# Kernel optimization log

Measured on AMD Instinct MI355X. Metric: run time of the kernel, lower is better.

Reference implementation:

```python
import jax, jax.numpy as jnp
import numpy as np

EPS = 1e-5  # matches torch default epsilon


def setup_inputs() -> dict:
    key = jax.random.key(0)
    ks = jax.random.split(key, 7)
    B, S, H = 32, 8192, 128
    return {
        "time_to_maturity": jax.random.uniform(ks[0], (B, S), jnp.float32),
        "log_moneyness": jax.random.normal(ks[1], (B, S), jnp.float32),
        "target_variance": jax.random.uniform(ks[2], (B, S), jnp.float32),
        "W1": jax.random.normal(ks[3], (2, H), jnp.float32) * 0.5,
        "b1": jax.random.normal(ks[4], (H,), jnp.float32) * 0.1,
        "W2": jax.random.normal(ks[5], (H,), jnp.float32) * 0.5,
        "b2": jax.random.normal(ks[6], (1,), jnp.float32) * 0.1,
    }


def reference(time_to_maturity, log_moneyness, target_variance, W1, b1, W2, b2):
    # Upstream surface model: elementwise (t, x) -> total implied variance w > 0.
    def w_fn(t, x):
        h = jnp.tanh(t * W1[0] + x * W1[1] + b1)  # [H]
        return jax.nn.softplus(jnp.dot(h, W2) + b2[0])  # scalar

    w_t_fn = jax.grad(w_fn, argnums=0)
    w_x_fn = jax.grad(w_fn, argnums=1)
    w_xx_fn = jax.grad(w_x_fn, argnums=1)

    tf = time_to_maturity.reshape(-1)   # [N] flattened query points
    xf = log_moneyness.reshape(-1)
    tgt = target_variance.reshape(-1)
    N = tf.shape[0]

    # Diagonal Jacobian entries: replaces the O(N^2) unit-vector autograd loop.
    w = jax.vmap(w_fn)(tf, xf)
    w_t = jax.vmap(w_t_fn)(tf, xf)
    w_x = jax.vmap(w_x_fn)(tf, xf)
    w_xx = jax.vmap(w_xx_fn)(tf, xf)

    percentage_error = (w - tgt) / (tgt + EPS)
    mspe = jnp.sum(percentage_error ** 2)

    calendar = jnp.sum(jnp.maximum(-w_t, 0.0) ** 2)

    # Durrleman butterfly condition g(x)
    g = (1.0 - xf * w_x / (2.0 * w)) ** 2 - (w_x / 4.0) * (1.0 / w + 0.25) + w_xx / 2.0
    butterfly = jnp.sum(jnp.maximum(-g, 0.0) ** 2)

    return jnp.stack([mspe, calendar, butterfly]) / N
```

## Files before the change

kernel.cpp:

```cpp
#include <hip/hip_runtime.h>
#include <cmath>

#define HDIM 128
typedef float f32x2 __attribute__((ext_vector_type(2)));

constexpr float EPSF = 1e-5f;
constexpr float K2L  = 2.8853900817779268f;
constexpr float INVK = 0.34657359027997264f;
constexpr float L2E  = 1.4426950408889634f;
constexpr float LN2  = 0.6931471805599453f;
constexpr float UXXS = -2.0f * INVK * INVK;

__device__ inline float fast_rcp(float x) { return __builtin_amdgcn_rcpf(x); }

__device__ inline float fast_exp2(float x) {
#if __has_builtin(__builtin_amdgcn_exp2f)
    return __builtin_amdgcn_exp2f(x);
#else
    float r; asm("v_exp_f32 %0, %1" : "=v"(r) : "v"(x)); return r;
#endif
}

__device__ inline float fast_log2(float x) {
#if __has_builtin(__builtin_amdgcn_logf)
    return __builtin_amdgcn_logf(x);
#else
    float r; asm("v_log_f32 %0, %1" : "=v"(r) : "v"(x)); return r;
#endif
}

__device__ inline f32x2 splat2(float v) { return (f32x2){v, v}; }

__device__ inline f32x2 pk_fma(f32x2 a, f32x2 b, f32x2 c) {
#if __has_builtin(__builtin_elementwise_fma)
    return __builtin_elementwise_fma(a, b, c);
#else
    f32x2 r; r.x = fmaf(a.x, b.x, c.x); r.y = fmaf(a.y, b.y, c.y); return r;
#endif
}

__device__ inline double wave_reduce(double v) {
    #pragma unroll
    for (int off = 32; off > 0; off >>= 1)
        v += __shfl_down(v, off, 64);
    return v;
}

__device__ inline void point_epilogue(float u, float ut, float ux, float uxxp,
                                      float x, float tgt,
                                      double& mspe, double& cal, double& bfly)
{
    const float q  = fast_exp2(-fabsf(u) * L2E);
    const float rp = fast_rcp(1.f + q);
    const float s  = (u >= 0.f) ? rp : q * rp;
    const float w_log  = fmaxf(u, 0.f) + LN2 * fast_log2(1.f + q);
    const float w_tail = q * fmaf(-0.5f, q, 1.f);
    const float w  = (u < -9.f) ? w_tail : w_log;

    const float utt  = ut * INVK;
    const float uxt  = ux * INVK;
    const float uxxt = uxxp * UXXS;
    const float w_t  = s * utt;
    const float w_x  = s * uxt;
    const float w_xx = fmaf(s * (1.f - s), uxt * uxt, s * uxxt);

    const float pe = (w - tgt) * fast_rcp(tgt + EPSF);
    mspe += (double)pe * (double)pe;

    const float ctm = fmaxf(-w_t, 0.f);
    cal += (double)ctm * (double)ctm;

    const float invw = fast_rcp(w);
    const float a1 = fmaf(-0.5f * x * w_x, invw, 1.f);
    const float g  = fmaf(0.5f, w_xx,
                     fmaf(a1, a1, -0.25f * w_x * (invw + 0.25f)));
    const float btm = fmaxf(-g, 0.f);
    bfly += (double)btm * (double)btm;
}

__global__ __launch_bounds__(256) void surf_loss_main(
    const float* __restrict__ tt, const float* __restrict__ xx,
    const float* __restrict__ tg,
    const float* __restrict__ W1, const float* __restrict__ b1,
    const float* __restrict__ W2, const float* __restrict__ b2,
    double* __restrict__ partials, int N)
{
    __shared__ float4 cs[HDIM];
    __shared__ double sred[3][4];
    const int tid = threadIdx.x;
    for (int i = tid; i < HDIM; i += 256) {
        cs[i] = make_float4(W1[i] * K2L, W1[HDIM + i] * K2L, b1[i] * K2L, W2[i]);
    }
    __syncthreads();
    const float b2v = b2[0];

    double mspe = 0.0, cal = 0.0, bfly = 0.0;

    const int npair = N >> 1;
    const f32x2* __restrict__ tt2 = (const f32x2*)tt;
    const f32x2* __restrict__ xx2 = (const f32x2*)xx;
    const f32x2* __restrict__ tg2 = (const f32x2*)tg;

    for (int p = blockIdx.x * 256 + tid; p < npair; p += gridDim.x * 256) {
        const f32x2 t2 = tt2[p], x2 = xx2[p], g2 = tg2[p];
        f32x2 u2   = splat2(b2v);
        f32x2 ut2  = splat2(0.f);
        f32x2 ux2  = splat2(0.f);
        f32x2 uxx2 = splat2(0.f);
        #pragma unroll 8
        for (int i = 0; i < HDIM; ++i) {
            const float4 c = cs[i];
            f32x2 zp = pk_fma(x2, splat2(c.y), splat2(c.z));
            zp = pk_fma(t2, splat2(c.x), zp);
            f32x2 e2; e2.x = fast_exp2(zp.x); e2.y = fast_exp2(zp.y);
            const f32x2 ep = e2 + splat2(1.f);
            f32x2 r2; r2.x = fast_rcp(ep.x); r2.y = fast_rcp(ep.y);
            const f32x2 th2 = pk_fma(splat2(-2.f), r2, splat2(1.f));
            const f32x2 d2  = pk_fma(-th2, th2, splat2(1.f));
            const f32x2 wd2 = splat2(c.w) * d2;
            u2   = pk_fma(splat2(c.w), th2, u2);
            ut2  = pk_fma(wd2, splat2(c.x), ut2);
            ux2  = pk_fma(wd2, splat2(c.y), ux2);
            const f32x2 wtc = (wd2 * th2) * splat2(c.y);
            uxx2 = pk_fma(wtc, splat2(c.y), uxx2);
        }
        point_epilogue(u2.x, ut2.x, ux2.x, uxx2.x, x2.x, g2.x, mspe, cal, bfly);
        point_epilogue(u2.y, ut2.y, ux2.y, uxx2.y, x2.y, g2.y, mspe, cal, bfly);
    }

    if ((N & 1) && blockIdx.x == 0 && tid == 0) {
        const int idx = N - 1;
        const float t = tt[idx], x = xx[idx], tgt = tg[idx];
        float u = b2v, ut = 0.f, ux = 0.f, uxx = 0.f;
        for (int i = 0; i < HDIM; ++i) {
            const float4 c = cs[i];
            const float zp = fmaf(t, c.x, fmaf(x, c.y, c.z));
            const float e  = fast_exp2(zp);
            const float r  = fast_rcp(e + 1.f);
            const float th = fmaf(-2.f, r, 1.f);
            const float d  = fmaf(-th, th, 1.f);
            const float wd = c.w * d;
            u   = fmaf(c.w, th, u);
            ut  = fmaf(wd, c.x, ut);
            ux  = fmaf(wd, c.y, ux);
            uxx = fmaf(wd * th * c.y, c.y, uxx);
        }
        point_epilogue(u, ut, ux, uxx, x, tgt, mspe, cal, bfly);
    }

    double v0 = wave_reduce(mspe), v1 = wave_reduce(cal), v2 = wave_reduce(bfly);
    const int wid = tid >> 6, lane = tid & 63;
    if (lane == 0) { sred[0][wid] = v0; sred[1][wid] = v1; sred[2][wid] = v2; }
    __syncthreads();
    if (tid == 0) {
        double a = 0, b = 0, c = 0;
        #pragma unroll
        for (int wv = 0; wv < 4; ++wv) { a += sred[0][wv]; b += sred[1][wv]; c += sred[2][wv]; }
        partials[blockIdx.x * 3 + 0] = a;
        partials[blockIdx.x * 3 + 1] = b;
        partials[blockIdx.x * 3 + 2] = c;
    }
}

__global__ __launch_bounds__(256) void surf_loss_final(
    const double* __restrict__ partials, int nblocks, float* __restrict__ out, int N)
{
    const int tid = threadIdx.x;
    double a = 0, b = 0, c = 0;
    for (int i = tid; i < nblocks; i += 256) {
        a += partials[i * 3 + 0];
        b += partials[i * 3 + 1];
        c += partials[i * 3 + 2];
    }
    a = wave_reduce(a); b = wave_reduce(b); c = wave_reduce(c);
    __shared__ double sred[3][4];
    const int wid = tid >> 6, lane = tid & 63;
    if (lane == 0) { sred[0][wid] = a; sred[1][wid] = b; sred[2][wid] = c; }
    __syncthreads();
    if (tid == 0) {
        const double inv = 1.0 / (double)N;
        double s0 = 0, s1 = 0, s2 = 0;
        #pragma unroll
        for (int wv = 0; wv < 4; ++wv) { s0 += sred[0][wv]; s1 += sred[1][wv]; s2 += sred[2][wv]; }
        out[0] = (float)(s0 * inv);
        out[1] = (float)(s1 * inv);
        out[2] = (float)(s2 * inv);
    }
}

extern "C" void kernel_launch(void* const* d_in, const int* in_sizes, int n_in,
                              void* d_out, int out_size, void* d_ws, size_t ws_size,
                              hipStream_t stream) {
    const float* tt = (const float*)d_in[0];
    const float* xx = (const float*)d_in[1];
    const float* tg = (const float*)d_in[2];
    const float* W1 = (const float*)d_in[3];
    const float* b1 = (const float*)d_in[4];
    const float* W2 = (const float*)d_in[5];
    const float* b2 = (const float*)d_in[6];
    const int N = in_sizes[0];

    const int npair = N >> 1;
    int blocks = (npair + 255) / 256;
    if (blocks < 1) blocks = 1;
    if (blocks > 1024) blocks = 1024;
    while ((size_t)blocks * 3 * sizeof(double) > ws_size && blocks > 1) blocks >>= 1;

    double* partials = (double*)d_ws;
    surf_loss_main<<<blocks, 256, 0, stream>>>(tt, xx, tg, W1, b1, W2, b2, partials, N);
    surf_loss_final<<<1, 256, 0, stream>>>(partials, blocks, (float*)d_out, N);
}
```

Measured before the change: 20.54 us.

## Split hidden dimension across lane pairs and fuse final reduction via atomic counter

Each pair of adjacent lanes now shares two points, with each lane evaluating half of the 128 hidden units for both points, and the partial sums are combined with xor shuffles. This doubles the thread count per point so the grid has more work items per block. The separate final-reduction kernel is replaced by a last-block-done pattern using an atomic counter, with a memset to reset it. The cost is extra shuffles and a memset launch in place of the second kernel launch.

New measurement: 35.89 us. 74.7% more time.

```diff
diff --git a/kernel.cpp b/kernel.cpp
--- a/kernel.cpp
+++ b/kernel.cpp
@@ -78,15 +78,17 @@
     bfly += (double)btm * (double)btm;
 }
 
-__global__ __launch_bounds__(256) void surf_loss_main(
+__global__ __launch_bounds__(256, 4) void surf_loss_fused(
     const float* __restrict__ tt, const float* __restrict__ xx,
     const float* __restrict__ tg,
     const float* __restrict__ W1, const float* __restrict__ b1,
     const float* __restrict__ W2, const float* __restrict__ b2,
-    double* __restrict__ partials, int N)
+    double* __restrict__ partials, unsigned* __restrict__ counter,
+    float* __restrict__ out, int N)
 {
     __shared__ float4 cs[HDIM];
     __shared__ double sred[3][4];
+    __shared__ int lastflag;
     const int tid = threadIdx.x;
     for (int i = tid; i < HDIM; i += 256) {
         cs[i] = make_float4(W1[i] * K2L, W1[HDIM + i] * K2L, b1[i] * K2L, W2[i]);
@@ -96,42 +98,56 @@
 
     double mspe = 0.0, cal = 0.0, bfly = 0.0;
 
-    const int npair = N >> 1;
+    const int Ne = N & ~1;
     const f32x2* __restrict__ tt2 = (const f32x2*)tt;
     const f32x2* __restrict__ xx2 = (const f32x2*)xx;
     const f32x2* __restrict__ tg2 = (const f32x2*)tg;
 
-    for (int p = blockIdx.x * 256 + tid; p < npair; p += gridDim.x * 256) {
-        const f32x2 t2 = tt2[p], x2 = xx2[p], g2 = tg2[p];
-        f32x2 u2   = splat2(b2v);
+    const int h    = tid & 1;
+    const int coff = h << 6;
+
+    for (int g = blockIdx.x * 256 + tid; g < Ne; g += gridDim.x * 256) {
+        const int p = g >> 1;
+        const f32x2 tv = tt2[p], xv = xx2[p], gv = tg2[p];
+        f32x2 u2   = splat2(0.f);
         f32x2 ut2  = splat2(0.f);
         f32x2 ux2  = splat2(0.f);
         f32x2 uxx2 = splat2(0.f);
-        #pragma unroll 8
-        for (int i = 0; i < HDIM; ++i) {
-            const float4 c = cs[i];
-            f32x2 zp = pk_fma(x2, splat2(c.y), splat2(c.z));
-            zp = pk_fma(t2, splat2(c.x), zp);
-            f32x2 e2; e2.x = fast_exp2(zp.x); e2.y = fast_exp2(zp.y);
-            const f32x2 ep = e2 + splat2(1.f);
-            f32x2 r2; r2.x = fast_rcp(ep.x); r2.y = fast_rcp(ep.y);
-            const f32x2 th2 = pk_fma(splat2(-2.f), r2, splat2(1.f));
-            const f32x2 d2  = pk_fma(-th2, th2, splat2(1.f));
-            const f32x2 wd2 = splat2(c.w) * d2;
-            u2   = pk_fma(splat2(c.w), th2, u2);
-            ut2  = pk_fma(wd2, splat2(c.x), ut2);
-            ux2  = pk_fma(wd2, splat2(c.y), ux2);
-            const f32x2 wtc = (wd2 * th2) * splat2(c.y);
+        #pragma unroll 4
+        for (int i = 0; i < HDIM / 2; ++i) {
+            const float4 c = cs[i + coff];
+            const f32x2 z  = pk_fma(tv, splat2(c.x),
+                              pk_fma(xv, splat2(c.y), splat2(c.z)));
+            f32x2 e;  e.x = fast_exp2(z.x); e.y = fast_exp2(z.y);
+            const f32x2 ep = e + splat2(1.f);
+            f32x2 r;  r.x = fast_rcp(ep.x); r.y = fast_rcp(ep.y);
+            const f32x2 th = pk_fma(splat2(-2.f), r, splat2(1.f));
+            const f32x2 d  = pk_fma(-th, th, splat2(1.f));
+            const f32x2 wd = d * splat2(c.w);
+            u2   = pk_fma(th, splat2(c.w), u2);
+            ut2  = pk_fma(wd, splat2(c.x), ut2);
+            ux2  = pk_fma(wd, splat2(c.y), ux2);
+            const f32x2 wt  = wd * th;
+            const f32x2 wtc = wt * splat2(c.y);
             uxx2 = pk_fma(wtc, splat2(c.y), uxx2);
         }
-        point_epilogue(u2.x, ut2.x, ux2.x, uxx2.x, x2.x, g2.x, mspe, cal, bfly);
-        point_epilogue(u2.y, ut2.y, ux2.y, uxx2.y, x2.y, g2.y, mspe, cal, bfly);
+        u2.x   += __shfl_xor(u2.x,   1, 64);  u2.y   += __shfl_xor(u2.y,   1, 64);
+        ut2.x  += __shfl_xor(ut2.x,  1, 64);  ut2.y  += __shfl_xor(ut2.y,  1, 64);
+        ux2.x  += __shfl_xor(ux2.x,  1, 64);  ux2.y  += __shfl_xor(ux2.y,  1, 64);
+        uxx2.x += __shfl_xor(uxx2.x, 1, 64);  uxx2.y += __shfl_xor(uxx2.y, 1, 64);
+        const float u    = (h ? u2.y   : u2.x) + b2v;
+        const float ut   =  h ? ut2.y  : ut2.x;
+        const float ux   =  h ? ux2.y  : ux2.x;
+        const float uxxp =  h ? uxx2.y : uxx2.x;
+        const float xs   =  h ? xv.y   : xv.x;
+        const float tgs  =  h ? gv.y   : gv.x;
+        point_epilogue(u, ut, ux, uxxp, xs, tgs, mspe, cal, bfly);
     }
 
     if ((N & 1) && blockIdx.x == 0 && tid == 0) {
         const int idx = N - 1;
         const float t = tt[idx], x = xx[idx], tgt = tg[idx];
-        float u = b2v, ut = 0.f, ux = 0.f, uxx = 0.f;
+        float u = 0.f, ut = 0.f, ux = 0.f, uxx = 0.f;
         for (int i = 0; i < HDIM; ++i) {
             const float4 c = cs[i];
             const float zp = fmaf(t, c.x, fmaf(x, c.y, c.z));
@@ -145,7 +161,7 @@
             ux  = fmaf(wd, c.y, ux);
             uxx = fmaf(wd * th * c.y, c.y, uxx);
         }
-        point_epilogue(u, ut, ux, uxx, x, tgt, mspe, cal, bfly);
+        point_epilogue(u + b2v, ut, ux, uxx, x, tgt, mspe, cal, bfly);
     }
 
     double v0 = wave_reduce(mspe), v1 = wave_reduce(cal), v2 = wave_reduce(bfly);
@@ -159,32 +175,32 @@
         partials[blockIdx.x * 3 + 0] = a;
         partials[blockIdx.x * 3 + 1] = b;
         partials[blockIdx.x * 3 + 2] = c;
-    }
-}
-
-__global__ __launch_bounds__(256) void surf_loss_final(
-    const double* __restrict__ partials, int nblocks, float* __restrict__ out, int N)
-{
-    const int tid = threadIdx.x;
-    double a = 0, b = 0, c = 0;
-    for (int i = tid; i < nblocks; i += 256) {
-        a += partials[i * 3 + 0];
-        b += partials[i * 3 + 1];
-        c += partials[i * 3 + 2];
-    }
-    a = wave_reduce(a); b = wave_reduce(b); c = wave_reduce(c);
-    __shared__ double sred[3][4];
-    const int wid = tid >> 6, lane = tid & 63;
-    if (lane == 0) { sred[0][wid] = a; sred[1][wid] = b; sred[2][wid] = c; }
+        const unsigned old = __hip_atomic_fetch_add(counter, 1u,
+                                __ATOMIC_ACQ_REL, __HIP_MEMORY_SCOPE_AGENT);
+        lastflag = (old == gridDim.x - 1) ? 1 : 0;
+    }
     __syncthreads();
-    if (tid == 0) {
-        const double inv = 1.0 / (double)N;
-        double s0 = 0, s1 = 0, s2 = 0;
-        #pragma unroll
-        for (int wv = 0; wv < 4; ++wv) { s0 += sred[0][wv]; s1 += sred[1][wv]; s2 += sred[2][wv]; }
-        out[0] = (float)(s0 * inv);
-        out[1] = (float)(s1 * inv);
-        out[2] = (float)(s2 * inv);
+
+    if (lastflag) {
+        double a = 0, b = 0, c = 0;
+        const int nb = (int)gridDim.x;
+        for (int i = tid; i < nb; i += 256) {
+            a += __hip_atomic_load(&partials[i * 3 + 0], __ATOMIC_RELAXED, __HIP_MEMORY_SCOPE_AGENT);
+            b += __hip_atomic_load(&partials[i * 3 + 1], __ATOMIC_RELAXED, __HIP_MEMORY_SCOPE_AGENT);
+            c += __hip_atomic_load(&partials[i * 3 + 2], __ATOMIC_RELAXED, __HIP_MEMORY_SCOPE_AGENT);
+        }
+        a = wave_reduce(a); b = wave_reduce(b); c = wave_reduce(c);
+        if (lane == 0) { sred[0][wid] = a; sred[1][wid] = b; sred[2][wid] = c; }
+        __syncthreads();
+        if (tid == 0) {
+            const double inv = 1.0 / (double)N;
+            double s0 = 0, s1 = 0, s2 = 0;
+            #pragma unroll
+            for (int wv = 0; wv < 4; ++wv) { s0 += sred[0][wv]; s1 += sred[1][wv]; s2 += sred[2][wv]; }
+            out[0] = (float)(s0 * inv);
+            out[1] = (float)(s1 * inv);
+            out[2] = (float)(s2 * inv);
+        }
     }
 }
 
@@ -200,13 +216,15 @@
     const float* b2 = (const float*)d_in[6];
     const int N = in_sizes[0];
 
-    const int npair = N >> 1;
-    int blocks = (npair + 255) / 256;
+    int blocks = (N + 255) / 256;
     if (blocks < 1) blocks = 1;
     if (blocks > 1024) blocks = 1024;
-    while ((size_t)blocks * 3 * sizeof(double) > ws_size && blocks > 1) blocks >>= 1;
-
-    double* partials = (double*)d_ws;
-    surf_loss_main<<<blocks, 256, 0, stream>>>(tt, xx, tg, W1, b1, W2, b2, partials, N);
-    surf_loss_final<<<1, 256, 0, stream>>>(partials, blocks, (float*)d_out, N);
-}
+    while (32 + (size_t)blocks * 3 * sizeof(double) > ws_size && blocks > 1) blocks >>= 1;
+
+    unsigned* counter = (unsigned*)d_ws;
+    double* partials  = (double*)((char*)d_ws + 32);
+
+    hipMemsetAsync(d_ws, 0, 32, stream);
+    surf_loss_fused<<<blocks, 256, 0, stream>>>(tt, xx, tg, W1, b1, W2, b2,
+                                                partials, counter, (float*)d_out, N);
+}
```

## Reformulate tanh-MLP derivative sums in sigmoid form and share one reciprocal per pair

Applied to the files above, without the earlier changes.

Rewrites the hidden-unit loop in terms of r = 1/(1+e^z), using th = 1-2r and 1-th^2 = 4r(1-r). Weight products and the bias sum are precomputed into a second shared-memory table, so the inner loop runs fewer dependent ops. The two reciprocals per point pair become one reciprocal of the product plus two multiplies, cutting transcendental-unit pressure. It also adds an occupancy hint to launch bounds. The risks are overflow or underflow in ep.x*ep.y for large z, extra LDS reads per iteration, and changed rounding.

Result: slower. 21.19 us (+3.1%).

```diff
diff --git a/kernel.cpp b/kernel.cpp
--- a/kernel.cpp
+++ b/kernel.cpp
@@ -6,10 +6,8 @@
 
 constexpr float EPSF = 1e-5f;
 constexpr float K2L  = 2.8853900817779268f;
-constexpr float INVK = 0.34657359027997264f;
 constexpr float L2E  = 1.4426950408889634f;
 constexpr float LN2  = 0.6931471805599453f;
-constexpr float UXXS = -2.0f * INVK * INVK;
 
 __device__ inline float fast_rcp(float x) { return __builtin_amdgcn_rcpf(x); }
 
@@ -46,7 +44,7 @@
     return v;
 }
 
-__device__ inline void point_epilogue(float u, float ut, float ux, float uxxp,
+__device__ inline void point_epilogue(float u, float ut, float ux, float uxx,
                                       float x, float tgt,
                                       double& mspe, double& cal, double& bfly)
 {
@@ -57,12 +55,9 @@
     const float w_tail = q * fmaf(-0.5f, q, 1.f);
     const float w  = (u < -9.f) ? w_tail : w_log;
 
-    const float utt  = ut * INVK;
-    const float uxt  = ux * INVK;
-    const float uxxt = uxxp * UXXS;
-    const float w_t  = s * utt;
-    const float w_x  = s * uxt;
-    const float w_xx = fmaf(s * (1.f - s), uxt * uxt, s * uxxt);
+    const float w_t  = s * ut;
+    const float w_x  = s * ux;
+    const float w_xx = fmaf(s * (1.f - s), ux * ux, s * uxx);
 
     const float pe = (w - tgt) * fast_rcp(tgt + EPSF);
     mspe += (double)pe * (double)pe;
@@ -78,21 +73,31 @@
     bfly += (double)btm * (double)btm;
 }
 
-__global__ __launch_bounds__(256) void surf_loss_main(
+__global__ __launch_bounds__(256, 4) void surf_loss_main(
     const float* __restrict__ tt, const float* __restrict__ xx,
     const float* __restrict__ tg,
     const float* __restrict__ W1, const float* __restrict__ b1,
     const float* __restrict__ W2, const float* __restrict__ b2,
     double* __restrict__ partials, int N)
 {
-    __shared__ float4 cs[HDIM];
+    __shared__ float4 cs1[HDIM];
+    __shared__ float4 cs2[HDIM];
     __shared__ double sred[3][4];
+    __shared__ float vsum_s;
     const int tid = threadIdx.x;
     for (int i = tid; i < HDIM; i += 256) {
-        cs[i] = make_float4(W1[i] * K2L, W1[HDIM + i] * K2L, b1[i] * K2L, W2[i]);
-    }
-    __syncthreads();
-    const float b2v = b2[0];
+        const float a = W1[i], c = W1[HDIM + i], b = b1[i], v = W2[i];
+        cs1[i] = make_float4(K2L * a, K2L * c, K2L * b, v);
+        cs2[i] = make_float4(v * a, v * c, v * c * c, 0.f);
+    }
+    __syncthreads();
+    if (tid == 0) {
+        float s = 0.f;
+        for (int i = 0; i < HDIM; ++i) s += cs1[i].w;
+        vsum_s = s;
+    }
+    __syncthreads();
+    const float ubias = b2[0] + vsum_s;
 
     double mspe = 0.0, cal = 0.0, bfly = 0.0;
 
@@ -103,49 +108,53 @@
 
     for (int p = blockIdx.x * 256 + tid; p < npair; p += gridDim.x * 256) {
         const f32x2 t2 = tt2[p], x2 = xx2[p], g2 = tg2[p];
-        f32x2 u2   = splat2(b2v);
-        f32x2 ut2  = splat2(0.f);
-        f32x2 ux2  = splat2(0.f);
-        f32x2 uxx2 = splat2(0.f);
+        f32x2 S1  = splat2(0.f);
+        f32x2 AT  = splat2(0.f);
+        f32x2 AX  = splat2(0.f);
+        f32x2 AXX = splat2(0.f);
         #pragma unroll 8
         for (int i = 0; i < HDIM; ++i) {
-            const float4 c = cs[i];
-            f32x2 zp = pk_fma(x2, splat2(c.y), splat2(c.z));
-            zp = pk_fma(t2, splat2(c.x), zp);
-            f32x2 e2; e2.x = fast_exp2(zp.x); e2.y = fast_exp2(zp.y);
-            const f32x2 ep = e2 + splat2(1.f);
-            f32x2 r2; r2.x = fast_rcp(ep.x); r2.y = fast_rcp(ep.y);
-            const f32x2 th2 = pk_fma(splat2(-2.f), r2, splat2(1.f));
-            const f32x2 d2  = pk_fma(-th2, th2, splat2(1.f));
-            const f32x2 wd2 = splat2(c.w) * d2;
-            u2   = pk_fma(splat2(c.w), th2, u2);
-            ut2  = pk_fma(wd2, splat2(c.x), ut2);
-            ux2  = pk_fma(wd2, splat2(c.y), ux2);
-            const f32x2 wtc = (wd2 * th2) * splat2(c.y);
-            uxx2 = pk_fma(wtc, splat2(c.y), uxx2);
+            const float4 k1 = cs1[i];
+            const float4 k2 = cs2[i];
+            const f32x2 z  = pk_fma(t2, splat2(k1.x),
+                              pk_fma(x2, splat2(k1.y), splat2(k1.z)));
+            f32x2 e;  e.x = fast_exp2(z.x); e.y = fast_exp2(z.y);
+            const f32x2 ep = e + splat2(1.f);
+            const float R  = fast_rcp(ep.x * ep.y);
+            f32x2 r;  r.x = R * ep.y;  r.y = R * ep.x;
+            const f32x2 rr = pk_fma(-r, r, r);
+            const f32x2 th = pk_fma(splat2(-2.f), r, splat2(1.f));
+            const f32x2 s  = rr * th;
+            S1  = pk_fma(splat2(k1.w), r,  S1);
+            AT  = pk_fma(splat2(k2.x), rr, AT);
+            AX  = pk_fma(splat2(k2.y), rr, AX);
+            AXX = pk_fma(splat2(k2.z), s,  AXX);
         }
-        point_epilogue(u2.x, ut2.x, ux2.x, uxx2.x, x2.x, g2.x, mspe, cal, bfly);
-        point_epilogue(u2.y, ut2.y, ux2.y, uxx2.y, x2.y, g2.y, mspe, cal, bfly);
+        point_epilogue(fmaf(-2.f, S1.x, ubias), 4.f * AT.x, 4.f * AX.x, -8.f * AXX.x,
+                       x2.x, g2.x, mspe, cal, bfly);
+        point_epilogue(fmaf(-2.f, S1.y, ubias), 4.f * AT.y, 4.f * AX.y, -8.f * AXX.y,
+                       x2.y, g2.y, mspe, cal, bfly);
     }
 
     if ((N & 1) && blockIdx.x == 0 && tid == 0) {
         const int idx = N - 1;
         const float t = tt[idx], x = xx[idx], tgt = tg[idx];
-        float u = b2v, ut = 0.f, ux = 0.f, uxx = 0.f;
+        float S1 = 0.f, AT = 0.f, AX = 0.f, AXX = 0.f;
         for (int i = 0; i < HDIM; ++i) {
-            const float4 c = cs[i];
-            const float zp = fmaf(t, c.x, fmaf(x, c.y, c.z));
-            const float e  = fast_exp2(zp);
+            const float4 k1 = cs1[i];
+            const float4 k2 = cs2[i];
+            const float z  = fmaf(t, k1.x, fmaf(x, k1.y, k1.z));
+            const float e  = fast_exp2(z);
             const float r  = fast_rcp(e + 1.f);
+            const float rr = fmaf(-r, r, r);
             const float th = fmaf(-2.f, r, 1.f);
-            const float d  = fmaf(-th, th, 1.f);
-            const float wd = c.w * d;
-            u   = fmaf(c.w, th, u);
-            ut  = fmaf(wd, c.x, ut);
-            ux  = fmaf(wd, c.y, ux);
-            uxx = fmaf(wd * th * c.y, c.y, uxx);
+            S1  = fmaf(k1.w, r,  S1);
+            AT  = fmaf(k2.x, rr, AT);
+            AX  = fmaf(k2.y, rr, AX);
+            AXX = fmaf(k2.z, rr * th, AXX);
         }
-        point_epilogue(u, ut, ux, uxx, x, tgt, mspe, cal, bfly);
+        point_epilogue(fmaf(-2.f, S1, ubias), 4.f * AT, 4.f * AX, -8.f * AXX,
+                       x, tgt, mspe, cal, bfly);
     }
 
     double v0 = wave_reduce(mspe), v1 = wave_reduce(cal), v2 = wave_reduce(bfly);
```
